# Kernel optimization log

Hardware: AMD Instinct MI355X
Metric: run time of the kernel (lower is better)

The kernel has to match this reference:

```python
import jax, jax.numpy as jnp
import numpy as np

N_NODES = 100000

def setup_inputs() -> dict:
    key = jax.random.key(0)
    k = jax.random.split(key, 6)
    N, E, D = N_NODES, 1600000, 128
    x = jax.random.normal(k[0], (N, D), dtype=jnp.float32)
    edge_src = jax.random.randint(k[1], (E,), 0, N, dtype=jnp.int32)
    edge_dst = jax.random.randint(k[2], (E,), 0, N, dtype=jnp.int32)
    edge_weight = jax.random.uniform(k[3], (E,), dtype=jnp.float32)
    W1 = jax.random.normal(k[4], (D, D), dtype=jnp.float32) * (1.0 / np.sqrt(D))
    W2 = jax.random.normal(k[5], (D, D), dtype=jnp.float32) * (1.0 / np.sqrt(D))
    return {"x": x, "edge_src": edge_src, "edge_dst": edge_dst,
            "edge_weight": edge_weight, "W1": W1, "W2": W2}

def _graph_conv(x, W, src, dst, ew, n_nodes):
    # GraphConv: h = A @ (x @ W); A given as weighted edge list.
    h = x @ W                               # [N, D_out]
    msg = h[src] * ew[:, None]              # [E, D_out] gather + scale
    return jax.ops.segment_sum(msg, dst, num_segments=n_nodes)  # [N, D_out]

def reference(x, edge_src, edge_dst, edge_weight, W1, W2):
    n = x.shape[0]
    # layer 1: tanh(GraphConv) ; Dropout(0) is identity
    x = jnp.tanh(_graph_conv(x, W1, edge_src, edge_dst, edge_weight, n))
    # layer 2
    x = jnp.tanh(_graph_conv(x, W2, edge_src, edge_dst, edge_weight, n))
    return x
```

## Files before the change

kernel.cpp:

```cpp
#include <hip/hip_runtime.h>
#include <hip/hip_bf16.h>

#define N_NODES 100000
#define N_EDGES 1600000
#define D 128
#define BSZ 128
#define NBUCK 782
#define EPW 8192
#define NWG1 ((N_EDGES + EPW - 1) / EPW)
#define CAP 4096
#define OTS 272

typedef unsigned int  uint4n  __attribute__((ext_vector_type(4)));
typedef float         float4n __attribute__((ext_vector_type(4)));
typedef _Float16      half8n  __attribute__((ext_vector_type(8)));
typedef _Float16      half4n  __attribute__((ext_vector_type(4)));

#define SWZ(row, kb) (((row) << 8) + ((kb) ^ (((row) & 15) << 4)))

__device__ __forceinline__ float fast_tanh(float x) {
    float t = __builtin_amdgcn_exp2f(x * 2.885390081777927f);
    return 1.0f - 2.0f * __builtin_amdgcn_rcpf(t + 1.0f);
}

__global__ __launch_bounds__(256) void k_wprep(const float* __restrict__ W1,
                                               const float* __restrict__ W2,
                                               char* __restrict__ Wt,
                                               int* __restrict__ bcnt) {
    if (blockIdx.x == 32) {
        for (int i = threadIdx.x; i < NBUCK; i += 256) bcnt[i] = 0;
        return;
    }
    const float* W = (blockIdx.x < 16) ? W1 : W2;
    char* dst = Wt + ((blockIdx.x < 16) ? 0 : 32768);
    int t = (blockIdx.x & 15) * 256 + threadIdx.x;
    int idx = t * 4;
    int k = idx >> 7, c = idx & 127;
    float4 wv = *(const float4*)&W[idx];
    *(_Float16*)(dst + SWZ(c + 0, k * 2)) = (_Float16)wv.x;
    *(_Float16*)(dst + SWZ(c + 1, k * 2)) = (_Float16)wv.y;
    *(_Float16*)(dst + SWZ(c + 2, k * 2)) = (_Float16)wv.z;
    *(_Float16*)(dst + SWZ(c + 3, k * 2)) = (_Float16)wv.w;
}


__global__ __launch_bounds__(256) void k_hist1(const int* __restrict__ dst,
                                               int* __restrict__ bcnt) {
    __shared__ int h[NBUCK];
    for (int i = threadIdx.x; i < NBUCK; i += 256) h[i] = 0;
    __syncthreads();
    int base = blockIdx.x * EPW;
    int end  = min(base + EPW, N_EDGES);
    for (int i = base + threadIdx.x; i < end; i += 256)
        atomicAdd(&h[dst[i] >> 7], 1);
    __syncthreads();
    for (int i = threadIdx.x; i < NBUCK; i += 256)
        if (h[i]) atomicAdd(&bcnt[i], h[i]);
}

__global__ void k_scanN(const int* __restrict__ bcnt, int* __restrict__ boff,
                        int* __restrict__ gcur) {
    __shared__ int tmp[256];
    int tid = threadIdx.x;
    int carry = 0;
    for (int c = 0; c < (NBUCK + 255) / 256; c++) {
        int i = c * 256 + tid;
        int v = (i < NBUCK) ? bcnt[i] : 0;
        tmp[tid] = v;
        __syncthreads();
        int run = v;
        for (int off = 1; off < 256; off <<= 1) {
            int t = (tid >= off) ? tmp[tid - off] : 0;
            __syncthreads();
            run += t;
            tmp[tid] = run;
            __syncthreads();
        }
        int excl = carry + run - v;
        if (i < NBUCK) { boff[i] = excl; gcur[i] = excl; }
        int tot = tmp[255];
        __syncthreads();
        carry += tot;
    }
    if (tid == 0) boff[NBUCK] = N_EDGES;
}

__global__ __launch_bounds__(256) void k_scat1(const int* __restrict__ src,
                                               const int* __restrict__ dst,
                                               const float* __restrict__ ew,
                                               int* __restrict__ gcur,
                                               int2* __restrict__ ebuf) {
    __shared__ int h[NBUCK];
    __shared__ int rb[NBUCK];
    for (int i = threadIdx.x; i < NBUCK; i += 256) h[i] = 0;
    __syncthreads();
    int base = blockIdx.x * EPW;
    int end  = min(base + EPW, N_EDGES);
    for (int i = base + threadIdx.x; i < end; i += 256)
        atomicAdd(&h[dst[i] >> 7], 1);
    __syncthreads();
    for (int i = threadIdx.x; i < NBUCK; i += 256) {
        int c = h[i];
        if (c) rb[i] = atomicAdd(&gcur[i], c);
    }
    __syncthreads();
    for (int i = base + threadIdx.x; i < end; i += 256) {
        int d  = dst[i];
        int bk = d >> 7;
        int p  = atomicAdd(&rb[bk], 1);
        ebuf[p] = make_int2((src[i] << 8) | (d & 127), __float_as_int(ew[i]));
    }
}

__global__ __launch_bounds__(512) void k_sortb(int2* __restrict__ ebuf,
                                               const int* __restrict__ boff,
                                               int* __restrict__ rowptr) {
    __shared__ int2 se[CAP];
    __shared__ int cnt[BSZ];
    __shared__ int cur[BSZ];
    int tid = threadIdx.x;
    int b   = blockIdx.x;
    int e0 = boff[b], e1 = boff[b + 1];
    int m  = e1 - e0;
    if (tid < BSZ) cnt[tid] = 0;
    __syncthreads();
    int2 ovf;
    bool hasOvf = false;
    for (int i = tid; i < m; i += 512) {
        int2 v = ebuf[e0 + i];
        if (i < CAP) se[i] = v;
        else { ovf = v; hasOvf = true; }
        atomicAdd(&cnt[v.x & (BSZ - 1)], 1);
    }
    __syncthreads();
    if (tid < 64) {
        int a  = cnt[tid * 2], bq = cnt[tid * 2 + 1];
        int s  = a + bq;
        int incl = s;
        #pragma unroll
        for (int off = 1; off < 64; off <<= 1) {
            int t = __shfl_up(incl, off, 64);
            if (tid >= off) incl += t;
        }
        int ex = incl - s;
        cur[tid * 2]     = ex;
        cur[tid * 2 + 1] = ex + a;
        int node = b * BSZ + tid * 2;
        if (node     <= N_NODES) rowptr[node]     = e0 + ex;
        if (node + 1 <= N_NODES) rowptr[node + 1] = e0 + ex + a;
    }
    __syncthreads();
    for (int i = tid; i < m && i < CAP; i += 512) {
        int2 v = se[i];
        int p = atomicAdd(&cur[v.x & (BSZ - 1)], 1);
        ebuf[e0 + p] = v;
    }
    if (hasOvf) {
        int p = atomicAdd(&cur[ovf.x & (BSZ - 1)], 1);
        ebuf[e0 + p] = ovf;
    }
}

template<bool XF16>
__global__ __launch_bounds__(256) void k_gemm(const void* __restrict__ Xv,
                                              const char* __restrict__ Wt,
                                              _Float16* __restrict__ H, int n) {
    __shared__ char smem[17408];
    char* sA = smem;
    int tid  = threadIdx.x;
    int lane = tid & 63, w = tid >> 6;
    int rows0 = blockIdx.x * 64;

    int rb = (w >> 1) * 32;
    int cb = (w & 1) * 64;
    int lr = lane & 15;
    int kg = (lane >> 4) * 16;

    if (XF16) {
        const _Float16* Xh = (const _Float16*)Xv;
        #pragma unroll
        for (int rep = 0; rep < 4; rep++) {
            int ef = rep * 2048 + tid * 8;
            int r = ef >> 7, c = ef & 127;
            int rg = rows0 + r;
            half8n v = half8n(0);
            if (rg < n) v = *(const half8n*)(Xh + (size_t)rg * 128 + c);
            *(half8n*)(sA + SWZ(r, c * 2)) = v;
        }
    } else {
        const float* Xf = (const float*)Xv;
        #pragma unroll
        for (int rep = 0; rep < 8; rep++) {
            int ef = rep * 1024 + tid * 4;
            int r = ef >> 7, c = ef & 127;
            int rg = rows0 + r;
            float4 xv = make_float4(0.f, 0.f, 0.f, 0.f);
            if (rg < n) xv = *(const float4*)(Xf + (size_t)rg * 128 + c);
            half4n hv;
            hv[0] = (_Float16)xv.x; hv[1] = (_Float16)xv.y;
            hv[2] = (_Float16)xv.z; hv[3] = (_Float16)xv.w;
            *(half4n*)(sA + SWZ(r, c * 2)) = hv;
        }
    }
    __syncthreads();

    float4n acc[2][4] = {};
    #pragma unroll
    for (int ks = 0; ks < 4; ks++) {
        half8n bwk[4];
        #pragma unroll
        for (int ct = 0; ct < 4; ct++)
            bwk[ct] = *(const half8n*)(Wt + SWZ(cb + ct * 16 + lr, ks * 64 + kg));
        half8n af[2];
        #pragma unroll
        for (int rt = 0; rt < 2; rt++)
            af[rt] = *(const half8n*)(sA + SWZ(rb + rt * 16 + lr, ks * 64 + kg));
        #pragma unroll
        for (int rt = 0; rt < 2; rt++)
            #pragma unroll
            for (int ct = 0; ct < 4; ct++)
                acc[rt][ct] = __builtin_amdgcn_mfma_f32_16x16x32_f16(af[rt], bwk[ct], acc[rt][ct], 0, 0, 0);
    }

    __syncthreads();
    char* OT = smem;
    int rloc = rb + (lane >> 4) * 4;
    #pragma unroll
    for (int rt = 0; rt < 2; rt++) {
        #pragma unroll
        for (int ct = 0; ct < 4; ct++) {
            int col = cb + ct * 16 + lr;
            #pragma unroll
            for (int r = 0; r < 4; r++)
                *(_Float16*)(OT + (rloc + rt * 16 + r) * OTS + col * 2) = (_Float16)acc[rt][ct][r];
        }
    }
    __syncthreads();
    #pragma unroll
    for (int rep = 0; rep < 4; rep++) {
        int ef = rep * 2048 + tid * 8;
        int r = ef >> 7, c = ef & 127;
        int rg = rows0 + r;
        if (rg < n) {
            half8n v = *(const half8n*)(OT + r * OTS + c * 2);
            *(half8n*)&H[(size_t)rg * 128 + c] = v;
        }
    }
}

template<bool OUTF16>
__global__ __launch_bounds__(256) void k_agg(const _Float16* __restrict__ H,
                                             const int* __restrict__ rowptr,
                                             const int2* __restrict__ ebuf,
                                             void* __restrict__ outv, int n) {
    int wv   = (blockIdx.x * 256 + threadIdx.x) >> 6;
    int lane = threadIdx.x & 63;
    int g = lane >> 4;
    int c = lane & 15;
    int node = wv * 4 + g;
    if (node >= n) return;
    const char* Hc = (const char*)H + (c << 4);
    int e0 = rowptr[node], e1 = rowptr[node + 1];
    float acc[8] = {};
    int e = e0;
    for (; e + 4 <= e1; e += 4) {
        int2 d0 = ebuf[e];
        int2 d1 = ebuf[e + 1];
        int2 d2 = ebuf[e + 2];
        int2 d3 = ebuf[e + 3];
        half8n v0 = *(const half8n*)(Hc + (size_t)((unsigned)d0.x & 0xFFFFFF00u));
        half8n v1 = *(const half8n*)(Hc + (size_t)((unsigned)d1.x & 0xFFFFFF00u));
        half8n v2 = *(const half8n*)(Hc + (size_t)((unsigned)d2.x & 0xFFFFFF00u));
        half8n v3 = *(const half8n*)(Hc + (size_t)((unsigned)d3.x & 0xFFFFFF00u));
        float w0 = __int_as_float(d0.y);
        float w1 = __int_as_float(d1.y);
        float w2 = __int_as_float(d2.y);
        float w3 = __int_as_float(d3.y);
        #pragma unroll
        for (int j = 0; j < 8; j++) acc[j] = __builtin_fmaf((float)v0[j], w0, acc[j]);
        #pragma unroll
        for (int j = 0; j < 8; j++) acc[j] = __builtin_fmaf((float)v1[j], w1, acc[j]);
        #pragma unroll
        for (int j = 0; j < 8; j++) acc[j] = __builtin_fmaf((float)v2[j], w2, acc[j]);
        #pragma unroll
        for (int j = 0; j < 8; j++) acc[j] = __builtin_fmaf((float)v3[j], w3, acc[j]);
    }
    for (; e < e1; ++e) {
        int2 ed = ebuf[e];
        half8n v = *(const half8n*)(Hc + (size_t)((unsigned)ed.x & 0xFFFFFF00u));
        float w = __int_as_float(ed.y);
        #pragma unroll
        for (int j = 0; j < 8; j++) acc[j] = __builtin_fmaf((float)v[j], w, acc[j]);
    }
    if (OUTF16) {
        half8n hv;
        #pragma unroll
        for (int j = 0; j < 8; j++) hv[j] = (_Float16)fast_tanh(acc[j]);
        *(uint4n*)((_Float16*)outv + (size_t)node * 128 + c * 8) = *(uint4n*)&hv;
    } else {
        float* op = (float*)outv + (size_t)node * 128 + c * 8;
        float4n o0, o1;
        o0.x = fast_tanh(acc[0]); o0.y = fast_tanh(acc[1]);
        o0.z = fast_tanh(acc[2]); o0.w = fast_tanh(acc[3]);
        o1.x = fast_tanh(acc[4]); o1.y = fast_tanh(acc[5]);
        o1.z = fast_tanh(acc[6]); o1.w = fast_tanh(acc[7]);
        __builtin_nontemporal_store(o0, (float4n*)op);
        __builtin_nontemporal_store(o1, (float4n*)(op + 4));
    }
}


extern "C" void kernel_launch(void* const* d_in, const int* in_sizes, int n_in,
                              void* d_out, int out_size, void* d_ws, size_t ws_size,
                              hipStream_t stream) {
    const float* x    = (const float*)d_in[0];
    const int*   esrc = (const int*)d_in[1];
    const int*   edst = (const int*)d_in[2];
    const float* ew   = (const float*)d_in[3];
    const float* W1   = (const float*)d_in[4];
    const float* W2   = (const float*)d_in[5];
    float* out = (float*)d_out;

    _Float16* hbuf = (_Float16*)d_ws;
    _Float16* act1 = hbuf + (size_t)N_NODES * D;
    int2* ebuf     = (int2*)(act1 + (size_t)N_NODES * D);
    int*  bcnt     = (int*)(ebuf + N_EDGES);
    int*  boff     = bcnt + NBUCK;
    int*  gcur     = boff + (NBUCK + 1);
    int*  rowptr   = gcur + NBUCK;
    char* Wt       = (char*)(rowptr + N_NODES + 8);
    (void)ws_size; (void)in_sizes; (void)n_in; (void)out_size;

    k_wprep<<<33, 256, 0, stream>>>(W1, W2, Wt, bcnt);
    k_hist1<<<NWG1, 256, 0, stream>>>(edst, bcnt);
    k_scanN<<<1, 256, 0, stream>>>(bcnt, boff, gcur);
    k_scat1<<<NWG1, 256, 0, stream>>>(esrc, edst, ew, gcur, ebuf);
    k_sortb<<<NBUCK, 512, 0, stream>>>(ebuf, boff, rowptr);

    int gemm_blocks = (N_NODES + 63) / 64;
    int agg_blocks  = (N_NODES + 15) / 16;

    k_gemm<false><<<gemm_blocks, 256, 0, stream>>>(x, Wt, hbuf, N_NODES);
    k_agg<true><<<agg_blocks, 256, 0, stream>>>(hbuf, rowptr, ebuf, act1, N_NODES);
    k_gemm<true><<<gemm_blocks, 256, 0, stream>>>(act1, Wt + 32768, hbuf, N_NODES);
    k_agg<false><<<agg_blocks, 256, 0, stream>>>(hbuf, rowptr, ebuf, out, N_NODES);
}
```

Before: 226.1 us.

## Split feature matrix into two column planes and aggregate each plane separately

Stores the projected features and the intermediate activations as two planes of 64 columns each. Aggregation launches a second grid dimension so each pass gathers only one half-row per edge. The intent is a smaller random-gather working set per pass, for better cache hit rates. In exchange, the edge list and row pointers are read twice, and each gather is half as wide.

```diff
diff --git a/kernel.cpp b/kernel.cpp
--- a/kernel.cpp
+++ b/kernel.cpp
@@ -10,6 +10,7 @@
 #define NWG1 ((N_EDGES + EPW - 1) / EPW)
 #define CAP 4096
 #define OTS 272
+#define PLANE ((size_t)N_NODES * 64)
 
 typedef unsigned int  uint4n  __attribute__((ext_vector_type(4)));
 typedef float         float4n __attribute__((ext_vector_type(4)));
@@ -184,7 +185,8 @@
             int r = ef >> 7, c = ef & 127;
             int rg = rows0 + r;
             half8n v = half8n(0);
-            if (rg < n) v = *(const half8n*)(Xh + (size_t)rg * 128 + c);
+            if (rg < n)
+                v = *(const half8n*)(Xh + (size_t)(c >> 6) * PLANE + (size_t)rg * 64 + (c & 63));
             *(half8n*)(sA + SWZ(r, c * 2)) = v;
         }
     } else {
@@ -243,7 +245,7 @@
         int rg = rows0 + r;
         if (rg < n) {
             half8n v = *(const half8n*)(OT + r * OTS + c * 2);
-            *(half8n*)&H[(size_t)rg * 128 + c] = v;
+            *(half8n*)(H + (size_t)(c >> 6) * PLANE + (size_t)rg * 64 + (c & 63)) = v;
         }
     }
 }
@@ -255,57 +257,55 @@
                                              void* __restrict__ outv, int n) {
     int wv   = (blockIdx.x * 256 + threadIdx.x) >> 6;
     int lane = threadIdx.x & 63;
+    int pass = blockIdx.y;
     int g = lane >> 4;
     int c = lane & 15;
     int node = wv * 4 + g;
     if (node >= n) return;
-    const char* Hc = (const char*)H + (c << 4);
+    const char* Hc = (const char*)(H + (size_t)pass * PLANE) + c * 8;
     int e0 = rowptr[node], e1 = rowptr[node + 1];
-    float acc[8] = {};
+    float acc[4] = {};
     int e = e0;
     for (; e + 4 <= e1; e += 4) {
         int2 d0 = ebuf[e];
         int2 d1 = ebuf[e + 1];
         int2 d2 = ebuf[e + 2];
         int2 d3 = ebuf[e + 3];
-        half8n v0 = *(const half8n*)(Hc + (size_t)((unsigned)d0.x & 0xFFFFFF00u));
-        half8n v1 = *(const half8n*)(Hc + (size_t)((unsigned)d1.x & 0xFFFFFF00u));
-        half8n v2 = *(const half8n*)(Hc + (size_t)((unsigned)d2.x & 0xFFFFFF00u));
-        half8n v3 = *(const half8n*)(Hc + (size_t)((unsigned)d3.x & 0xFFFFFF00u));
+        half4n v0 = *(const half4n*)(Hc + ((size_t)((unsigned)d0.x & 0xFFFFFF00u) >> 1));
+        half4n v1 = *(const half4n*)(Hc + ((size_t)((unsigned)d1.x & 0xFFFFFF00u) >> 1));
+        half4n v2 = *(const half4n*)(Hc + ((size_t)((unsigned)d2.x & 0xFFFFFF00u) >> 1));
+        half4n v3 = *(const half4n*)(Hc + ((size_t)((unsigned)d3.x & 0xFFFFFF00u) >> 1));
         float w0 = __int_as_float(d0.y);
         float w1 = __int_as_float(d1.y);
         float w2 = __int_as_float(d2.y);
         float w3 = __int_as_float(d3.y);
         #pragma unroll
-        for (int j = 0; j < 8; j++) acc[j] = __builtin_fmaf((float)v0[j], w0, acc[j]);
-        #pragma unroll
-        for (int j = 0; j < 8; j++) acc[j] = __builtin_fmaf((float)v1[j], w1, acc[j]);
-        #pragma unroll
-        for (int j = 0; j < 8; j++) acc[j] = __builtin_fmaf((float)v2[j], w2, acc[j]);
-        #pragma unroll
-        for (int j = 0; j < 8; j++) acc[j] = __builtin_fmaf((float)v3[j], w3, acc[j]);
+        for (int j = 0; j < 4; j++) acc[j] = __builtin_fmaf((float)v0[j], w0, acc[j]);
+        #pragma unroll
+        for (int j = 0; j < 4; j++) acc[j] = __builtin_fmaf((float)v1[j], w1, acc[j]);
+        #pragma unroll
+        for (int j = 0; j < 4; j++) acc[j] = __builtin_fmaf((float)v2[j], w2, acc[j]);
+        #pragma unroll
+        for (int j = 0; j < 4; j++) acc[j] = __builtin_fmaf((float)v3[j], w3, acc[j]);
     }
     for (; e < e1; ++e) {
         int2 ed = ebuf[e];
-        half8n v = *(const half8n*)(Hc + (size_t)((unsigned)ed.x & 0xFFFFFF00u));
+        half4n v = *(const half4n*)(Hc + ((size_t)((unsigned)ed.x & 0xFFFFFF00u) >> 1));
         float w = __int_as_float(ed.y);
         #pragma unroll
-        for (int j = 0; j < 8; j++) acc[j] = __builtin_fmaf((float)v[j], w, acc[j]);
+        for (int j = 0; j < 4; j++) acc[j] = __builtin_fmaf((float)v[j], w, acc[j]);
     }
     if (OUTF16) {
-        half8n hv;
-        #pragma unroll
-        for (int j = 0; j < 8; j++) hv[j] = (_Float16)fast_tanh(acc[j]);
-        *(uint4n*)((_Float16*)outv + (size_t)node * 128 + c * 8) = *(uint4n*)&hv;
+        half4n hv;
+        #pragma unroll
+        for (int j = 0; j < 4; j++) hv[j] = (_Float16)fast_tanh(acc[j]);
+        *(half4n*)((_Float16*)outv + (size_t)pass * PLANE + (size_t)node * 64 + c * 4) = hv;
     } else {
-        float* op = (float*)outv + (size_t)node * 128 + c * 8;
-        float4n o0, o1;
-        o0.x = fast_tanh(acc[0]); o0.y = fast_tanh(acc[1]);
-        o0.z = fast_tanh(acc[2]); o0.w = fast_tanh(acc[3]);
-        o1.x = fast_tanh(acc[4]); o1.y = fast_tanh(acc[5]);
-        o1.z = fast_tanh(acc[6]); o1.w = fast_tanh(acc[7]);
-        __builtin_nontemporal_store(o0, (float4n*)op);
-        __builtin_nontemporal_store(o1, (float4n*)(op + 4));
+        float4n o;
+        o.x = fast_tanh(acc[0]); o.y = fast_tanh(acc[1]);
+        o.z = fast_tanh(acc[2]); o.w = fast_tanh(acc[3]);
+        __builtin_nontemporal_store(o,
+            (float4n*)((float*)outv + (size_t)node * 128 + pass * 64 + c * 4));
     }
 }
 
@@ -322,8 +322,8 @@
     float* out = (float*)d_out;
 
     _Float16* hbuf = (_Float16*)d_ws;
-    _Float16* act1 = hbuf + (size_t)N_NODES * D;
-    int2* ebuf     = (int2*)(act1 + (size_t)N_NODES * D);
+    _Float16* act1 = hbuf + 2 * PLANE;
+    int2* ebuf     = (int2*)(act1 + 2 * PLANE);
     int*  bcnt     = (int*)(ebuf + N_EDGES);
     int*  boff     = bcnt + NBUCK;
     int*  gcur     = boff + (NBUCK + 1);
@@ -338,10 +338,10 @@
     k_sortb<<<NBUCK, 512, 0, stream>>>(ebuf, boff, rowptr);
 
     int gemm_blocks = (N_NODES + 63) / 64;
-    int agg_blocks  = (N_NODES + 15) / 16;
+    dim3 gga((N_NODES + 15) / 16, 2);
 
     k_gemm<false><<<gemm_blocks, 256, 0, stream>>>(x, Wt, hbuf, N_NODES);
-    k_agg<true><<<agg_blocks, 256, 0, stream>>>(hbuf, rowptr, ebuf, act1, N_NODES);
+    k_agg<true><<<gga, 256, 0, stream>>>(hbuf, rowptr, ebuf, act1, N_NODES);
     k_gemm<true><<<gemm_blocks, 256, 0, stream>>>(act1, Wt + 32768, hbuf, N_NODES);
-    k_agg<false><<<agg_blocks, 256, 0, stream>>>(hbuf, rowptr, ebuf, out, N_NODES);
-}
+    k_agg<false><<<gga, 256, 0, stream>>>(hbuf, rowptr, ebuf, out, N_NODES);
+}
```

Measured after the change: 231.2 us. 1.02x slower.
